# Performance work log

Hardware: AMD Instinct MI355X
Metric: run time of the kernel (lower is better)

Reference implementation:

```python
import jax, jax.numpy as jnp
import numpy as np

EPS = 1e-12

def _l2norm(v, axis):
    # matches torch F.normalize: divide by norm clamped to eps
    n = jnp.sqrt(jnp.sum(v * v, axis=axis, keepdims=True))
    return v / jnp.maximum(n, EPS)

def setup_inputs() -> dict:
    key = jax.random.key(0)
    k1, k2 = jax.random.split(key)
    B, C, S, D = 256, 1000, 4, 512
    x = jax.random.normal(k1, (B, D), dtype=jnp.float32)
    # xavier_uniform over [C, S, D]: fan_in = S*D? torch treats dims (S, D) pairwise; approximate with uniform bound
    bound = float(np.sqrt(6.0 / (S + D)))
    W = jax.random.uniform(k2, (C, S, D), dtype=jnp.float32, minval=-bound, maxval=bound)
    return {"x": x, "W": W}

def reference(x, W):
    xn = _l2norm(x, axis=1)            # [B, D]
    Wn = _l2norm(W, axis=2)            # [C, S, D]
    logits = jnp.einsum('bd,csd->bcs', xn, Wn)        # [B, C, S]
    x_proj = jnp.einsum('bcs,csd->bcd', logits, Wn)   # [B, C, D]
    x_proj = _l2norm(x_proj, axis=2)
    out = jnp.einsum('bd,bcd->bc', xn, x_proj)        # [B, C]
    return out
```

## Files before the change

kernel.cpp:

```cpp
#include <hip/hip_runtime.h>

#define B_ 256
#define C_ 1000
#define D_ 512

typedef __bf16 bf16x4 __attribute__((ext_vector_type(4)));
typedef __bf16 bf16x8 __attribute__((ext_vector_type(8)));
typedef float  f32x4  __attribute__((ext_vector_type(4)));

__device__ __forceinline__ bf16x8 cvt8(float4 a, float4 b) {
    bf16x8 r;
    r[0] = (__bf16)a.x; r[1] = (__bf16)a.y; r[2] = (__bf16)a.z; r[3] = (__bf16)a.w;
    r[4] = (__bf16)b.x; r[5] = (__bf16)b.y; r[6] = (__bf16)b.z; r[7] = (__bf16)b.w;
    return r;
}
__device__ __forceinline__ bf16x4 cvt4(float4 a) {
    bf16x4 r;
    r[0] = (__bf16)a.x; r[1] = (__bf16)a.y; r[2] = (__bf16)a.z; r[3] = (__bf16)a.w;
    return r;
}

__global__ __launch_bounds__(256) void k_packx(const float* __restrict__ x,
                                               __bf16* __restrict__ xf,
                                               float* __restrict__ invx) {
    int n = blockIdx.x * 256 + threadIdx.x;
    int r = n >> 6;
    int j = n & 63;
    const float* src = x + r * D_ + j * 8;
    float4 a = *(const float4*)src;
    float4 b = *(const float4*)(src + 4);
    int bt = r >> 4, l15 = r & 15, ks = j >> 2, quad = j & 3;
    int idx = ((bt * 16 + ks) * 4 + quad) * 16 + l15;
    *(bf16x8*)(xf + idx * 8) = cvt8(a, b);
    float sn = a.x*a.x + a.y*a.y + a.z*a.z + a.w*a.w
             + b.x*b.x + b.y*b.y + b.z*b.z + b.w*b.w;
    #pragma unroll
    for (int o = 32; o; o >>= 1) sn += __shfl_down(sn, o);
    if ((threadIdx.x & 63) == 0) invx[r] = 1.0f / fmaxf(sqrtf(sn), 1e-12f);
}

__global__ __launch_bounds__(256, 2) void k_main(const float* __restrict__ W,
                                                 const __bf16* __restrict__ xf,
                                                 const float* __restrict__ invx,
                                                 float* __restrict__ out) {
    __shared__ __align__(16) char smem[64 * 272];
    int blk = blockIdx.x;
    int ct = blk >> 1;
    int bh = blk & 1;
    int t = threadIdx.x;
    int lane = t & 63, wv = t >> 6;
    int l15 = lane & 15, quad = lane >> 4;

    const float* wbase = W + ct * 16 * D_;
    #pragma unroll
    for (int p = 0; p < 8; p++) {
        int ch = t + 256 * p;
        int row = ch >> 7, pos = ch & 127;
        float4 v = *(const float4*)(wbase + row * D_ + pos * 4);
        int ks = pos >> 3, qd = (pos >> 1) & 3, off = (pos & 1) * 4;
        *(bf16x4*)(smem + (ks * 4 + qd) * 272 + row * 16 + off * 2) = cvt4(v);
    }
    __syncthreads();

    int bt0 = bh * 8 + wv * 2;
    int bt1 = bt0 + 1;
    const bf16x8* xp0 = (const bf16x8*)xf + (bt0 * 64 + quad) * 16 + l15;
    const bf16x8* xp1 = (const bf16x8*)xf + (bt1 * 64 + quad) * 16 + l15;
    const char* lp = smem + quad * 272 + l15 * 16;

    f32x4 acc0 = {0.f, 0.f, 0.f, 0.f};
    f32x4 acc1 = {0.f, 0.f, 0.f, 0.f};
    f32x4 accg = {0.f, 0.f, 0.f, 0.f};
    #pragma unroll
    for (int ks = 0; ks < 16; ks++) {
        bf16x8 af = *(const bf16x8*)(lp + ks * 1088);
        bf16x8 b0 = xp0[ks * 64];
        bf16x8 b1 = xp1[ks * 64];
        acc0 = __builtin_amdgcn_mfma_f32_16x16x32_bf16(af, b0, acc0, 0, 0, 0);
        acc1 = __builtin_amdgcn_mfma_f32_16x16x32_bf16(af, b1, acc1, 0, 0, 0);
        accg = __builtin_amdgcn_mfma_f32_16x16x32_bf16(af, af, accg, 0, 0, 0);
    }

    float g[4][4];
    #pragma unroll
    for (int s = 0; s < 4; s++) {
        float v = accg[s];
        #pragma unroll
        for (int q = 0; q < 4; q++) g[s][q] = __shfl(v, 20 * quad + q);
    }
    float iv[4];
    #pragma unroll
    for (int s = 0; s < 4; s++) iv[s] = 1.0f / fmaxf(sqrtf(fmaxf(g[s][s], 0.f)), 1e-12f);

    #pragma unroll
    for (int sub = 0; sub < 2; sub++) {
        int bt = sub ? bt1 : bt0;
        f32x4 acc = sub ? acc1 : acc0;
        float ivx = invx[bt * 16 + l15];
        float l[4];
        #pragma unroll
        for (int s = 0; s < 4; s++) l[s] = acc[s] * ivx * iv[s];
        float num = l[0]*l[0] + l[1]*l[1] + l[2]*l[2] + l[3]*l[3];
        float den2 = 0.f;
        #pragma unroll
        for (int s = 0; s < 4; s++) {
            float r = 0.f;
            #pragma unroll
            for (int q = 0; q < 4; q++) r += g[s][q] * iv[q] * l[q];
            den2 += l[s] * iv[s] * r;
        }
        float den = fmaxf(sqrtf(fmaxf(den2, 0.f)), 1e-12f);
        float val = num / den;

        float4 o;
        o.x = __shfl(val, l15);
        o.y = __shfl(val, l15 + 16);
        o.z = __shfl(val, l15 + 32);
        o.w = __shfl(val, l15 + 48);
        if (quad == 0)
            *(float4*)(out + (bt * 16 + l15) * C_ + ct * 4) = o;
    }
}

extern "C" void kernel_launch(void* const* d_in, const int* in_sizes, int n_in,
                              void* d_out, int out_size, void* d_ws, size_t ws_size,
                              hipStream_t stream) {
    const float* x = (const float*)d_in[0];
    const float* W = (const float*)d_in[1];
    float* out = (float*)d_out;

    char* ws = (char*)d_ws;
    __bf16* xf  = (__bf16*)ws;
    float*  ivx = (float*)(ws + 524288);

    k_packx<<<64, 256, 0, stream>>>(x, xf, ivx);
    k_main<<<500, 256, 0, stream>>>(W, xf, ivx, out);
}
```

Measured before the change: 68.69 us.

## Fuse x packing and norm into main kernel using MFMA self-products

Removes the separate pack kernel for x. Each wave now loads its x rows straight from global fp32, converts them to bf16 in registers, and computes each row's squared norm with extra MFMA x·x products. The norm is read off the diagonal with a shuffle. Block indices are also remapped so that the two batch halves of a column tile are spaced eight blocks apart, which may change L2 sharing. This saves one launch and the workspace round trip, at the cost of more registers, redundant x loads across blocks, and a bf16-precision norm for x.

New measurement: 78.87 us. 14.8% more time.

```diff
diff --git a/kernel.cpp b/kernel.cpp
--- a/kernel.cpp
+++ b/kernel.cpp
@@ -1,6 +1,5 @@
 #include <hip/hip_runtime.h>
 
-#define B_ 256
 #define C_ 1000
 #define D_ 512
 
@@ -20,38 +19,21 @@
     return r;
 }
 
-__global__ __launch_bounds__(256) void k_packx(const float* __restrict__ x,
-                                               __bf16* __restrict__ xf,
-                                               float* __restrict__ invx) {
-    int n = blockIdx.x * 256 + threadIdx.x;
-    int r = n >> 6;
-    int j = n & 63;
-    const float* src = x + r * D_ + j * 8;
-    float4 a = *(const float4*)src;
-    float4 b = *(const float4*)(src + 4);
-    int bt = r >> 4, l15 = r & 15, ks = j >> 2, quad = j & 3;
-    int idx = ((bt * 16 + ks) * 4 + quad) * 16 + l15;
-    *(bf16x8*)(xf + idx * 8) = cvt8(a, b);
-    float sn = a.x*a.x + a.y*a.y + a.z*a.z + a.w*a.w
-             + b.x*b.x + b.y*b.y + b.z*b.z + b.w*b.w;
-    #pragma unroll
-    for (int o = 32; o; o >>= 1) sn += __shfl_down(sn, o);
-    if ((threadIdx.x & 63) == 0) invx[r] = 1.0f / fmaxf(sqrtf(sn), 1e-12f);
-}
+__global__ __launch_bounds__(256, 2) void k_fused(const float* __restrict__ x,
+                                                  const float* __restrict__ W,
+                                                  float* __restrict__ out) {
+    __shared__ __align__(16) char smem[64 * 272];
 
-__global__ __launch_bounds__(256, 2) void k_main(const float* __restrict__ W,
-                                                 const __bf16* __restrict__ xf,
-                                                 const float* __restrict__ invx,
-                                                 float* __restrict__ out) {
-    __shared__ __align__(16) char smem[64 * 272];
-    int blk = blockIdx.x;
-    int ct = blk >> 1;
-    int bh = blk & 1;
+    int bid = blockIdx.x;
+    int ct = (bid & 7) + ((bid >> 4) << 3);
+    int bh = (bid >> 3) & 1;
+    if (ct >= 250) return;
+
     int t = threadIdx.x;
     int lane = t & 63, wv = t >> 6;
     int l15 = lane & 15, quad = lane >> 4;
 
-    const float* wbase = W + ct * 16 * D_;
+    const float* wbase = W + ct * (16 * D_);
     #pragma unroll
     for (int p = 0; p < 8; p++) {
         int ch = t + 256 * p;
@@ -60,25 +42,37 @@
         int ks = pos >> 3, qd = (pos >> 1) & 3, off = (pos & 1) * 4;
         *(bf16x4*)(smem + (ks * 4 + qd) * 272 + row * 16 + off * 2) = cvt4(v);
     }
+
+    int bt0 = bh * 8 + wv * 2;
+    bf16x8 bf[2][16];
+    #pragma unroll
+    for (int lt = 0; lt < 2; lt++) {
+        const float* src = x + ((bt0 + lt) * 16 + l15) * D_ + quad * 8;
+        #pragma unroll
+        for (int ks = 0; ks < 16; ks++) {
+            float4 va = *(const float4*)(src + ks * 32);
+            float4 vb = *(const float4*)(src + ks * 32 + 4);
+            bf[lt][ks] = cvt8(va, vb);
+        }
+    }
     __syncthreads();
 
-    int bt0 = bh * 8 + wv * 2;
-    int bt1 = bt0 + 1;
-    const bf16x8* xp0 = (const bf16x8*)xf + (bt0 * 64 + quad) * 16 + l15;
-    const bf16x8* xp1 = (const bf16x8*)xf + (bt1 * 64 + quad) * 16 + l15;
     const char* lp = smem + quad * 272 + l15 * 16;
-
-    f32x4 acc0 = {0.f, 0.f, 0.f, 0.f};
-    f32x4 acc1 = {0.f, 0.f, 0.f, 0.f};
-    f32x4 accg = {0.f, 0.f, 0.f, 0.f};
+    f32x4 acc0  = {0.f, 0.f, 0.f, 0.f};
+    f32x4 acc1  = {0.f, 0.f, 0.f, 0.f};
+    f32x4 accg  = {0.f, 0.f, 0.f, 0.f};
+    f32x4 accx0 = {0.f, 0.f, 0.f, 0.f};
+    f32x4 accx1 = {0.f, 0.f, 0.f, 0.f};
     #pragma unroll
     for (int ks = 0; ks < 16; ks++) {
         bf16x8 af = *(const bf16x8*)(lp + ks * 1088);
-        bf16x8 b0 = xp0[ks * 64];
-        bf16x8 b1 = xp1[ks * 64];
-        acc0 = __builtin_amdgcn_mfma_f32_16x16x32_bf16(af, b0, acc0, 0, 0, 0);
-        acc1 = __builtin_amdgcn_mfma_f32_16x16x32_bf16(af, b1, acc1, 0, 0, 0);
-        accg = __builtin_amdgcn_mfma_f32_16x16x32_bf16(af, af, accg, 0, 0, 0);
+        bf16x8 b0 = bf[0][ks];
+        bf16x8 b1 = bf[1][ks];
+        acc0  = __builtin_amdgcn_mfma_f32_16x16x32_bf16(af, b0, acc0, 0, 0, 0);
+        acc1  = __builtin_amdgcn_mfma_f32_16x16x32_bf16(af, b1, acc1, 0, 0, 0);
+        accg  = __builtin_amdgcn_mfma_f32_16x16x32_bf16(af, af, accg, 0, 0, 0);
+        accx0 = __builtin_amdgcn_mfma_f32_16x16x32_bf16(b0, b0, accx0, 0, 0, 0);
+        accx1 = __builtin_amdgcn_mfma_f32_16x16x32_bf16(b1, b1, accx1, 0, 0, 0);
     }
 
     float g[4][4];
@@ -92,11 +86,18 @@
     #pragma unroll
     for (int s = 0; s < 4; s++) iv[s] = 1.0f / fmaxf(sqrtf(fmaxf(g[s][s], 0.f)), 1e-12f);
 
+    int sd = l15 & 3;
+    int srcl = ((l15 >> 2) << 4) + l15;
+
     #pragma unroll
     for (int sub = 0; sub < 2; sub++) {
-        int bt = sub ? bt1 : bt0;
+        int bt = bt0 + sub;
         f32x4 acc = sub ? acc1 : acc0;
-        float ivx = invx[bt * 16 + l15];
+        f32x4 ax  = sub ? accx1 : accx0;
+        float cand = (sd == 0) ? ax[0] : (sd == 1) ? ax[1] : (sd == 2) ? ax[2] : ax[3];
+        float dg = __shfl(cand, srcl);
+        float ivx = 1.0f / fmaxf(sqrtf(fmaxf(dg, 0.f)), 1e-12f);
+
         float l[4];
         #pragma unroll
         for (int s = 0; s < 4; s++) l[s] = acc[s] * ivx * iv[s];
@@ -129,10 +130,6 @@
     const float* W = (const float*)d_in[1];
     float* out = (float*)d_out;
 
-    char* ws = (char*)d_ws;
-    __bf16* xf  = (__bf16*)ws;
-    float*  ivx = (float*)(ws + 524288);
-
-    k_packx<<<64, 256, 0, stream>>>(x, xf, ivx);
-    k_main<<<500, 256, 0, stream>>>(W, xf, ivx, out);
+    (void)d_ws; (void)ws_size;
+    k_fused<<<512, 256, 0, stream>>>(x, W, out);
 }
```
